# Performance work log

Hardware: AMD Instinct MI355X
Metric: run time of the kernel (lower is better)

## Reference

```python
import jax, jax.numpy as jnp
import numpy as np
from jax import lax

N, L, B = 256, 20, 10      # batch, max_seq (baskets), max_bas (items/basket)
D, H, ASP, K = 128, 128, 4, 16  # dim, h, aspects, nbNUM
NITEMS = 20000
H2 = 2 * H


def setup_inputs() -> dict:
    key = jax.random.key(0)
    ks = jax.random.split(key, 20)
    nrm = lambda k, shape, s=0.05: (jax.random.normal(k, shape) * s).astype(jnp.float32)
    seq = jax.random.randint(ks[0], (N, L, B), 0, NITEMS + 1)          # indices into itemEmb
    uHis = jax.random.uniform(ks[1], (N, NITEMS), dtype=jnp.float32)   # dense user history
    itemEmb = nrm(ks[2], (NITEMS + 1, D), 0.1).at[0].set(0.0)          # padding_idx=0 row zeroed
    fc1_w = nrm(ks[3], (1, L * B * D)); fc1_b = jnp.zeros((1,), jnp.float32)
    aspProju = nrm(ks[4], (ASP, 1, H))
    aspProji = nrm(ks[5], (ASP, D, H))
    dh_w = nrm(ks[6], (H, D)); dh_b = jnp.zeros((H,), jnp.float32)
    wih0 = nrm(ks[7], (4 * H2, H2)); whh0 = nrm(ks[8], (4 * H2, H2))
    bih0 = jnp.zeros((4 * H2,), jnp.float32); bhh0 = jnp.zeros((4 * H2,), jnp.float32)
    wih1 = nrm(ks[9], (4 * H2, H2)); whh1 = nrm(ks[10], (4 * H2, H2))
    bih1 = jnp.zeros((4 * H2,), jnp.float32); bhh1 = jnp.zeros((4 * H2,), jnp.float32)
    out_w = nrm(ks[11], (NITEMS, H2)); out_b = jnp.zeros((NITEMS,), jnp.float32)
    his_w = nrm(ks[12], (H2, NITEMS)); his_b = jnp.zeros((H2,), jnp.float32)
    g1_w = nrm(ks[13], (1, H2)); g1_b = jnp.zeros((1,), jnp.float32)
    g2_w = nrm(ks[14], (1, H2)); g2_b = jnp.zeros((1,), jnp.float32)
    return dict(seq=seq, uHis=uHis, itemEmb=itemEmb, fc1_w=fc1_w, fc1_b=fc1_b,
                aspProju=aspProju, aspProji=aspProji, dh_w=dh_w, dh_b=dh_b,
                wih0=wih0, whh0=whh0, bih0=bih0, bhh0=bhh0,
                wih1=wih1, whh1=whh1, bih1=bih1, bhh1=bhh1,
                out_w=out_w, out_b=out_b, his_w=his_w, his_b=his_b,
                g1_w=g1_w, g1_b=g1_b, g2_w=g2_w, g2_b=g2_b)


def _lstm_layer(x, wih, whh, bih, bhh):
    # x: [N, T, in]; PyTorch gate order i, f, g, o
    Hs = whh.shape[1]
    def step(carry, xt):
        h, c = carry
        g = xt @ wih.T + bih + h @ whh.T + bhh
        i, f, gg, o = jnp.split(g, 4, axis=-1)
        c = jax.nn.sigmoid(f) * c + jax.nn.sigmoid(i) * jnp.tanh(gg)
        h = jax.nn.sigmoid(o) * jnp.tanh(c)
        return (h, c), h
    h0 = jnp.zeros((x.shape[0], Hs), x.dtype)
    _, ys = lax.scan(step, (h0, h0), jnp.swapaxes(x, 0, 1))
    return jnp.swapaxes(ys, 0, 1)


def reference(seq, uHis, itemEmb, fc1_w, fc1_b, aspProju, aspProji, dh_w, dh_b,
              wih0, whh0, bih0, bhh0, wih1, whh1, bih1, bhh1,
              out_w, out_b, his_w, his_b, g1_w, g1_b, g2_w, g2_b):
    n, l, b = seq.shape
    embs = itemEmb[seq]                                   # [N,L,B,D]
    # MIE_user: fresh fc1 -> scalar per user, project per aspect
    u_embs = embs.reshape(n, -1) @ fc1_w.T + fc1_b        # [N,1]
    userAsp = jnp.tanh(jnp.einsum('no,aoh->nah', u_embs, aspProju))      # [N,ASP,H]
    # MIE_item
    itemAsp = jnp.tanh(jnp.einsum('nlbd,adh->nalbh', embs, aspProji))    # [N,ASP,L,B,H]
    # SNA: per-aspect exact L2 kNN over the batch (FAISS IndexFlatL2 equivalent)
    uA = jnp.transpose(jnp.tanh(userAsp), (1, 0, 2))      # [ASP,N,H] (double tanh, as in source)
    sq = jnp.sum(uA * uA, -1)                             # [ASP,N]
    dist = sq[:, :, None] + sq[:, None, :] - 2.0 * jnp.einsum('anh,amh->anm', uA, uA)
    dist = jnp.where(jnp.eye(n, dtype=bool)[None], -1.0, dist)   # self ranked first
    _, I = lax.top_k(lax.stop_gradient(-dist), K)         # [ASP,N,K] ascending distance
    I = I[:, :, 1:]                                       # drop self -> K-1 neighbors
    # sum of neighbor embeddings via multiplicity matmul (== gather+sum)
    M = jax.nn.one_hot(I, n, dtype=embs.dtype).sum(2)     # [ASP,N,N]
    nb_sum = jnp.einsum('apn,nlbd->aplbd', M, embs)       # [ASP,N,L,B,D]
    nb_h = nb_sum @ dh_w.T + dh_b                         # [ASP,N,L,B,H]
    embs_PI = jnp.transpose(nb_h.sum(axis=3), (1, 0, 2, 3))        # [N,ASP,L,H]
    embs_UI = jnp.tanh(itemAsp).sum(axis=3)               # [N,ASP,L,H] (double tanh)
    neighbAsps = jnp.concatenate([embs_UI, embs_PI], axis=-1)      # [N,ASP,L,2H]
    # raw view (not permute!) then max-pool over last dim of size ASP
    x = jnp.reshape(neighbAsps, (n, l, H2, ASP)).max(axis=-1)      # [N,L,2H]
    # 2-layer LSTM (eval mode: inter-layer dropout inactive)
    y = _lstm_layer(x, wih0, whh0, bih0, bhh0)
    y = _lstm_layer(y, wih1, whh1, bih1, bhh1)
    h_agg = jnp.tanh(y.sum(axis=1))                       # [N,2H]
    probs = jax.nn.softmax(h_agg @ out_w.T + out_b, axis=-1)       # [N,NITEMS]
    uHis_h = uHis @ his_w.T + his_b                        # [N,2H]
    gate = jax.nn.sigmoid(uHis_h @ g1_w.T + g1_b + h_agg @ g2_w.T + g2_b)  # [N,1]
    scores = gate * probs + (1.0 - gate) * uHis
    return scores
```

## Files before the change

kernel.cpp:

```cpp
#include <hip/hip_runtime.h>
#include <math.h>

#define N_ 256
#define L_ 20
#define B_ 10
#define D_ 128
#define H_ 128
#define ASP_ 4
#define KK_ 16
#define NIT_ 20000
#define H2_ 256
#define G4_ 1024
#define LBD_ 25600
#define NL_ 5120
#define NLB_ 51200

typedef __attribute__((ext_vector_type(8))) short bf16x8;
typedef __attribute__((ext_vector_type(4))) short bf16x4;
typedef __attribute__((ext_vector_type(4))) float f32x4;

__device__ __forceinline__ float sigf_fast(float x){
  return __builtin_amdgcn_rcpf(1.0f + __expf(-x));
}
__device__ __forceinline__ float tanh_fast(float x){
  return 1.0f - 2.0f*__builtin_amdgcn_rcpf(__expf(2.0f*x) + 1.0f);
}
__device__ __forceinline__ unsigned short f2b(float f){
  unsigned int u = __float_as_uint(f);
  unsigned int r = (u + 0x7FFFu + ((u>>16)&1u)) >> 16;
  return (unsigned short)r;
}
__device__ __forceinline__ float b2f(unsigned short b){
  return __uint_as_float(((unsigned int)b) << 16);
}

__global__ void k_gather2(const int* __restrict__ seq, const float* __restrict__ itemEmb,
                          float* __restrict__ embs, unsigned short* __restrict__ ebh,
                          float* __restrict__ eb){
  int nl = blockIdx.x;
  int d = threadIdx.x;
  float s = 0.f;
  #pragma unroll
  for(int b=0;b<B_;b++){
    int idx = seq[nl*B_ + b];
    float v = itemEmb[(size_t)idx*D_ + d];
    embs[(size_t)(nl*B_+b)*D_ + d] = v;
    ebh[(size_t)(nl*B_+b)*D_ + d] = f2b(v);
    s += v;
  }
  eb[(size_t)nl*D_ + d] = s;
}

__global__ void k_fc1(const float* __restrict__ embs, const float* __restrict__ w,
                      const float* __restrict__ b, float* __restrict__ u){
  int n = blockIdx.x; int t = threadIdx.x;
  float s = 0.f;
  for (int i = t; i < LBD_; i += 256) s += embs[n*LBD_+i]*w[i];
  __shared__ float red[256];
  red[t]=s; __syncthreads();
  for (int o=128;o>0;o>>=1){ if(t<o) red[t]+=red[t+o]; __syncthreads(); }
  if(t==0) u[n]=red[0]+b[0];
}

__global__ void k_uasq(const float* __restrict__ u, const float* __restrict__ proju,
                       float* __restrict__ ua, float* __restrict__ sq){
  int an = blockIdx.x;
  int h = threadIdx.x;
  int a = an / N_, n = an % N_;
  float v = tanhf(tanhf(u[n]*proju[a*H_+h]));
  ua[an*H_ + h] = v;
  __shared__ float red[128];
  red[h] = v*v; __syncthreads();
  for(int o=64;o>0;o>>=1){ if(h<o) red[h]+=red[h+o]; __syncthreads(); }
  if(h==0) sq[an]=red[0];
}

__global__ __launch_bounds__(256) void k_disttopk(const float* __restrict__ ua,
    const float* __restrict__ sq, int* __restrict__ nbr){
  int n = blockIdx.x, a = blockIdx.y, m = threadIdx.x;
  __shared__ float un[H_];
  __shared__ float row[N_];
  if(m < H_) un[m] = ua[(a*N_+n)*H_ + m];
  __syncthreads();
  const float* um = &ua[(a*N_+m)*H_];
  float dot=0.f;
  for(int h=0;h<H_;h++) dot += un[h]*um[h];
  float dval = sq[a*N_+n] + sq[a*N_+m] - 2.f*dot;
  if(m==n) dval = -1.0f;
  row[m] = dval;
  __syncthreads();
  if(m < 64){
    int lane = m;
    int wid = a*N_+n;
    float v[4]; int idx[4];
    #pragma unroll
    for(int j=0;j<4;j++){ int mm = lane*4 + j; v[j] = row[mm]; idx[j] = mm; }
    for(int k=0;k<KK_;k++){
      float bv = v[0]; int bi = idx[0];
      #pragma unroll
      for(int j=1;j<4;j++)
        if(v[j] < bv || (v[j]==bv && idx[j] < bi)){ bv=v[j]; bi=idx[j]; }
      float rv = bv; int ri = bi;
      #pragma unroll
      for(int o=32;o>0;o>>=1){
        float ov = __shfl_xor(rv, o, 64);
        int   oi = __shfl_xor(ri, o, 64);
        if(ov < rv || (ov==rv && oi < ri)){ rv=ov; ri=oi; }
      }
      if((ri>>2) == lane){ v[ri&3] = 3.4e38f; idx[ri&3] = 0x7fffffff; }
      if(k>0 && lane==0) nbr[wid*(KK_-1)+(k-1)] = ri;
    }
  }
}

__global__ void k_prep(const float* __restrict__ wih0, const float* __restrict__ whh0,
                       const float* __restrict__ wih1, const float* __restrict__ whh1,
                       const float* __restrict__ bih0, const float* __restrict__ bhh0,
                       const float* __restrict__ bih1, const float* __restrict__ bhh1,
                       const float* __restrict__ proji,
                       float* __restrict__ wp0, unsigned short* __restrict__ whb0,
                       float* __restrict__ wp1, unsigned short* __restrict__ whb1,
                       float* __restrict__ bp0, float* __restrict__ bp1,
                       unsigned short* __restrict__ projb){
  int i = blockIdx.x*blockDim.x + threadIdx.x;
  if(i < 262144){
    int k=i%H2_, j=i/H2_, g=j/H2_, jj=j%H2_;
    wp0[(jj*4+g)*H2_+k] = wih0[i];
  } else if(i < 524288){
    int e=i-262144; int k=e%H2_, j=e/H2_, g=j/H2_, jj=j%H2_;
    whb0[(jj*4+g)*H2_+k] = f2b(whh0[e]);
  } else if(i < 786432){
    int e=i-524288; int k=e%H2_, j=e/H2_, g=j/H2_, jj=j%H2_;
    wp1[(jj*4+g)*H2_+k] = wih1[e];
  } else if(i < 1048576){
    int e=i-786432; int k=e%H2_, j=e/H2_, g=j/H2_, jj=j%H2_;
    whb1[(jj*4+g)*H2_+k] = f2b(whh1[e]);
  } else if(i < 1114112){
    int e=i-1048576; int h=e%H_, d=(e/H_)%D_, aa=e/(D_*H_);
    projb[(aa*H_+h)*D_+d] = f2b(proji[e]);
  } else if(i < 1115136){
    int j=i-1114112; int g=j/H2_, jj=j%H2_;
    bp0[jj*4+g] = bih0[j] + bhh0[j];
  } else if(i < 1116160){
    int j=i-1115136; int g=j/H2_, jj=j%H2_;
    bp1[jj*4+g] = bih1[j] + bhh1[j];
  }
}

__global__ __launch_bounds__(256) void k_uimm(const unsigned short* __restrict__ ebh,
                                              const unsigned short* __restrict__ projb,
                                              float* __restrict__ na){
  __shared__ char smem[53248];
  unsigned short* As = (unsigned short*)smem;
  unsigned short* Bs = (unsigned short*)(smem + 20480);
  float*          Cs = (float*)smem;

  int mb = blockIdx.x;
  int a  = blockIdx.y;
  int tid = threadIdx.x;

  const unsigned short* asrc = ebh + (size_t)mb*10240;
  #pragma unroll
  for(int t=0;t<5;t++){
    int c = tid + t*256;
    int row = c >> 4;
    *(bf16x8*)(As + 8*(c ^ (row&7))) = *(const bf16x8*)(asrc + 8*c);
  }
  const unsigned short* bsrc = projb + a*16384;
  #pragma unroll
  for(int t=0;t<8;t++){
    int c = tid + t*256;
    int row = c >> 4;
    *(bf16x8*)(Bs + 8*(c ^ (row&7))) = *(const bf16x8*)(bsrc + 8*c);
  }
  __syncthreads();

  int lane = tid & 63, wave = tid >> 6;
  int l15 = lane & 15, l4 = lane >> 4;
  f32x4 acc[5][2] = {};
  #pragma unroll
  for(int kk=0;kk<4;kk++){
    bf16x8 bfr[2];
    #pragma unroll
    for(int tc=0;tc<2;tc++){
      int h = (wave*2+tc)*16 + l15;
      int c = h*16 + kk*4 + l4;
      bfr[tc] = *(const bf16x8*)(Bs + 8*(c ^ (h&7)));
    }
    #pragma unroll
    for(int tr=0;tr<5;tr++){
      int R = tr*16 + l15;
      int c = R*16 + kk*4 + l4;
      bf16x8 afr = *(const bf16x8*)(As + 8*(c ^ (R&7)));
      acc[tr][0] = __builtin_amdgcn_mfma_f32_16x16x32_bf16(afr, bfr[0], acc[tr][0], 0,0,0);
      acc[tr][1] = __builtin_amdgcn_mfma_f32_16x16x32_bf16(afr, bfr[1], acc[tr][1], 0,0,0);
    }
  }
  __syncthreads();

  #pragma unroll
  for(int tr=0;tr<5;tr++)
    #pragma unroll
    for(int tc=0;tc<2;tc++){
      int col = (wave*2+tc)*16 + l15;
      #pragma unroll
      for(int r=0;r<4;r++){
        int R = tr*16 + l4*4 + r;
        Cs[R*128 + col] = tanh_fast(tanh_fast(acc[tr][tc][r]));
      }
    }
  __syncthreads();

  #pragma unroll
  for(int t=0;t<4;t++){
    int oi = t*256 + tid;
    int g = oi >> 7, col = oi & 127;
    float s = 0.f;
    const float* p = Cs + g*1280 + col;
    #pragma unroll
    for(int b=0;b<10;b++) s += p[b*128];
    int nl = mb*8 + g;
    int n = nl/L_, l = nl%L_;
    na[((size_t)(n*ASP_+a)*L_ + l)*H2_ + col] = s;
  }
}

__global__ __launch_bounds__(256) void k_uhismm(const float* __restrict__ U,
    const float* __restrict__ W, const float* __restrict__ bias, float* __restrict__ C){
  __shared__ unsigned short As[2048];
  __shared__ unsigned short Bs[2048];
  int tid = threadIdx.x;
  int m0 = blockIdx.y*64, n0 = blockIdx.x*64;
  int kb0 = blockIdx.z*800;
  int row = tid & 63, q = tid >> 6;
  int lane = tid & 63, wave = tid >> 6;
  int l15 = lane & 15, l4 = lane >> 4;
  int wr = (wave>>1)*32, wc = (wave&1)*32;
  f32x4 acc[2][2] = {};
  for(int s=0;s<25;s++){
    int k0 = kb0 + s*32 + q*8;
    {
      const float* pa = &U[(size_t)(m0+row)*NIT_ + k0];
      float4 a0 = *(const float4*)pa, a1 = *(const float4*)(pa+4);
      bf16x8 av;
      av[0]=f2b(a0.x); av[1]=f2b(a0.y); av[2]=f2b(a0.z); av[3]=f2b(a0.w);
      av[4]=f2b(a1.x); av[5]=f2b(a1.y); av[6]=f2b(a1.z); av[7]=f2b(a1.w);
      *(bf16x8*)(As + 8*tid) = av;
      const float* pb = &W[(size_t)(n0+row)*NIT_ + k0];
      float4 b0 = *(const float4*)pb, b1 = *(const float4*)(pb+4);
      bf16x8 bv;
      bv[0]=f2b(b0.x); bv[1]=f2b(b0.y); bv[2]=f2b(b0.z); bv[3]=f2b(b0.w);
      bv[4]=f2b(b1.x); bv[5]=f2b(b1.y); bv[6]=f2b(b1.z); bv[7]=f2b(b1.w);
      *(bf16x8*)(Bs + 8*tid) = bv;
    }
    __syncthreads();
    bf16x8 afr[2], bfr[2];
    #pragma unroll
    for(int mt=0;mt<2;mt++) afr[mt] = *(const bf16x8*)(As + 8*(l4*64 + wr + mt*16 + l15));
    #pragma unroll
    for(int nt=0;nt<2;nt++) bfr[nt] = *(const bf16x8*)(Bs + 8*(l4*64 + wc + nt*16 + l15));
    #pragma unroll
    for(int mt=0;mt<2;mt++)
      #pragma unroll
      for(int nt=0;nt<2;nt++)
        acc[mt][nt] = __builtin_amdgcn_mfma_f32_16x16x32_bf16(afr[mt], bfr[nt], acc[mt][nt], 0,0,0);
    __syncthreads();
  }
  #pragma unroll
  for(int mt=0;mt<2;mt++)
    #pragma unroll
    for(int nt=0;nt<2;nt++){
      int col = n0 + wc + nt*16 + l15;
      #pragma unroll
      for(int r=0;r<4;r++){
        int rw = m0 + wr + mt*16 + l4*4 + r;
        float v = acc[mt][nt][r];
        if(blockIdx.z==0) v += bias[col];
        atomicAdd(&C[rw*H2_ + col], v);
      }
    }
}

__global__ __launch_bounds__(256) void k_xgmm(const float* __restrict__ A_,
    const float* __restrict__ W, const float* __restrict__ bias,
    unsigned short* __restrict__ Cb){
  __shared__ unsigned short As[2048];
  __shared__ unsigned short Bs[2048];
  int tid = threadIdx.x;
  int n0 = blockIdx.x*64, m0 = blockIdx.y*64;
  int row = tid & 63, q = tid >> 6;
  int lane = tid & 63, wave = tid >> 6;
  int l15 = lane & 15, l4 = lane >> 4;
  int wr = (wave>>1)*32, wc = (wave&1)*32;
  f32x4 acc[2][2] = {};
  for(int s=0;s<8;s++){
    int k0 = s*32 + q*8;
    {
      const float* pa = &A_[(size_t)(m0+row)*H2_ + k0];
      float4 a0 = *(const float4*)pa, a1 = *(const float4*)(pa+4);
      bf16x8 av;
      av[0]=f2b(a0.x); av[1]=f2b(a0.y); av[2]=f2b(a0.z); av[3]=f2b(a0.w);
      av[4]=f2b(a1.x); av[5]=f2b(a1.y); av[6]=f2b(a1.z); av[7]=f2b(a1.w);
      *(bf16x8*)(As + 8*tid) = av;
      const float* pb = &W[(size_t)(n0+row)*H2_ + k0];
      float4 b0 = *(const float4*)pb, b1 = *(const float4*)(pb+4);
      bf16x8 bv;
      bv[0]=f2b(b0.x); bv[1]=f2b(b0.y); bv[2]=f2b(b0.z); bv[3]=f2b(b0.w);
      bv[4]=f2b(b1.x); bv[5]=f2b(b1.y); bv[6]=f2b(b1.z); bv[7]=f2b(b1.w);
      *(bf16x8*)(Bs + 8*tid) = bv;
    }
    __syncthreads();
    bf16x8 afr[2], bfr[2];
    #pragma unroll
    for(int mt=0;mt<2;mt++) afr[mt] = *(const bf16x8*)(As + 8*(l4*64 + wr + mt*16 + l15));
    #pragma unroll
    for(int nt=0;nt<2;nt++) bfr[nt] = *(const bf16x8*)(Bs + 8*(l4*64 + wc + nt*16 + l15));
    #pragma unroll
    for(int mt=0;mt<2;mt++)
      #pragma unroll
      for(int nt=0;nt<2;nt++)
        acc[mt][nt] = __builtin_amdgcn_mfma_f32_16x16x32_bf16(afr[mt], bfr[nt], acc[mt][nt], 0,0,0);
    __syncthreads();
  }
  #pragma unroll
  for(int mt=0;mt<2;mt++)
    #pragma unroll
    for(int nt=0;nt<2;nt++){
      int col = n0 + wc + nt*16 + l15;
      float bs = bias[col];
      #pragma unroll
      for(int r=0;r<4;r++){
        int rw = m0 + wr + mt*16 + l4*4 + r;
        Cb[(size_t)rw*G4_ + col] = f2b(acc[mt][nt][r] + bs);
      }
    }
}

__global__ __launch_bounds__(256) void k_logitsmm(const unsigned short* __restrict__ Ab,
    const float* __restrict__ Wf, const float* __restrict__ bias,
    float* __restrict__ C){
  int n0 = blockIdx.x*32;
  int tid = threadIdx.x;
  int lane = tid & 63, wave = tid >> 6;
  int l15 = lane & 15, l4 = lane >> 4;
  f32x4 acc[4][2] = {};
  #pragma unroll
  for(int kk=0;kk<8;kk++){
    int k0 = kk*32 + l4*8;
    bf16x8 bfr[2];
    #pragma unroll
    for(int nt=0;nt<2;nt++){
      const float* pb = &Wf[(size_t)(n0 + nt*16 + l15)*H2_ + k0];
      float4 b0 = *(const float4*)pb, b1 = *(const float4*)(pb+4);
      bf16x8 bv;
      bv[0]=f2b(b0.x); bv[1]=f2b(b0.y); bv[2]=f2b(b0.z); bv[3]=f2b(b0.w);
      bv[4]=f2b(b1.x); bv[5]=f2b(b1.y); bv[6]=f2b(b1.z); bv[7]=f2b(b1.w);
      bfr[nt] = bv;
    }
    #pragma unroll
    for(int mt=0;mt<4;mt++){
      bf16x8 afr = *(const bf16x8*)(Ab + (size_t)(wave*64 + mt*16 + l15)*H2_ + k0);
      acc[mt][0] = __builtin_amdgcn_mfma_f32_16x16x32_bf16(afr, bfr[0], acc[mt][0], 0,0,0);
      acc[mt][1] = __builtin_amdgcn_mfma_f32_16x16x32_bf16(afr, bfr[1], acc[mt][1], 0,0,0);
    }
  }
  #pragma unroll
  for(int mt=0;mt<4;mt++)
    #pragma unroll
    for(int nt=0;nt<2;nt++){
      int col = n0 + nt*16 + l15;
      float bs = bias[col];
      #pragma unroll
      for(int r=0;r<4;r++){
        int row = wave*64 + mt*16 + l4*4 + r;
        C[(size_t)row*NIT_ + col] = acc[mt][nt][r] + bs;
      }
    }
}

__global__ __launch_bounds__(256) void k_gemm(const float* __restrict__ A, const float* __restrict__ W,
    float* __restrict__ C, const float* __restrict__ bias,
    int M, int Nn, int K, int kchunk, int atomic_mode){
  __shared__ float As[64][17];
  __shared__ float Ws[64][17];
  int tid = threadIdx.x;
  int tx = tid & 15, ty = tid >> 4;
  int m0 = blockIdx.y*64, n0 = blockIdx.x*64;
  int kb0 = blockIdx.z*kchunk;
  int kend = kb0 + kchunk; if(kend > K) kend = K;
  float acc[4][4] = {};
  int lrow = tid >> 2;
  int lc4 = (tid & 3) * 4;
  for(int kb = kb0; kb < kend; kb += 16){
    {
      int gr = m0 + lrow;
      float4 v = make_float4(0,0,0,0);
      if(gr < M) v = *(const float4*)&A[(long)gr*K + kb + lc4];
      As[lrow][lc4+0]=v.x; As[lrow][lc4+1]=v.y; As[lrow][lc4+2]=v.z; As[lrow][lc4+3]=v.w;
      int gw = n0 + lrow;
      float4 u = make_float4(0,0,0,0);
      if(gw < Nn) u = *(const float4*)&W[(long)gw*K + kb + lc4];
      Ws[lrow][lc4+0]=u.x; Ws[lrow][lc4+1]=u.y; Ws[lrow][lc4+2]=u.z; Ws[lrow][lc4+3]=u.w;
    }
    __syncthreads();
    for(int k=0;k<16;k++){
      float av[4], wv[4];
      #pragma unroll
      for(int r=0;r<4;r++) av[r]=As[ty*4+r][k];
      #pragma unroll
      for(int c=0;c<4;c++) wv[c]=Ws[tx*4+c][k];
      #pragma unroll
      for(int r=0;r<4;r++)
        #pragma unroll
        for(int c=0;c<4;c++) acc[r][c] += av[r]*wv[c];
    }
    __syncthreads();
  }
  for(int r=0;r<4;r++){
    int row = m0 + ty*4 + r; if(row >= M) continue;
    for(int c=0;c<4;c++){
      int col = n0 + tx*4 + c; if(col >= Nn) continue;
      float v = acc[r][c];
      if(bias && blockIdx.z==0) v += bias[col];
      if(atomic_mode) atomicAdd(&C[(long)row*Nn+col], v);
      else C[(long)row*Nn+col] = v;
    }
  }
}

__global__ void k_pi(const float* __restrict__ e2, const int* __restrict__ nbr,
                     const float* __restrict__ dh_b, float* __restrict__ na){
  int n = blockIdx.x, a = blockIdx.y, h = threadIdx.x;
  __shared__ int nb[KK_-1];
  if(h < KK_-1) nb[h] = nbr[(a*N_+n)*(KK_-1)+h];
  __syncthreads();
  float bias = (float)B_ * dh_b[h];
  for(int l=0;l<L_;l++){
    float s = bias;
    for(int k=0;k<KK_-1;k++) s += e2[(long)(nb[k]*L_ + l)*H_ + h];
    na[((long)(n*ASP_+a)*L_ + l)*H2_ + H_ + h] = s;
  }
}

__global__ void k_xmax(const float* __restrict__ na, float* __restrict__ x){
  int i = blockIdx.x*blockDim.x + threadIdx.x;
  if(i >= N_*L_*H2_) return;
  int n = i / (L_*H2_);
  int j = i % (L_*H2_);
  const float* p = &na[(long)n*ASP_*L_*H2_ + 4*j];
  x[i] = fmaxf(fmaxf(p[0],p[1]), fmaxf(p[2],p[3]));
}

__global__ __launch_bounds__(1024) void k_lstm_layer(
    const unsigned short* __restrict__ Whb,
    const unsigned short* __restrict__ xgb,
    float* __restrict__ Y){
  __shared__ unsigned short wc[65536];
  __shared__ unsigned short hs[2][16*H2_];
  int tid = threadIdx.x;
  int n0 = blockIdx.x * 16;
  int lane = tid & 63, wave = tid >> 6;
  int l15 = lane & 15, l4 = lane >> 4;
  int n = n0 + l15;
  float creg[4] = {0.f,0.f,0.f,0.f};
  {
    int ct0 = wave*4;
    #pragma unroll
    for(int it=0; it<8; it++){
      int c = it*64 + lane;
      int row = c >> 5;
      bf16x8 w8 = *(const bf16x8*)(Whb + (size_t)(ct0*16+row)*H2_ + (c&31)*8);
      *(bf16x8*)(wc + 8*((wave<<9) + (c ^ (row&7)))) = w8;
    }
  }
  const unsigned short* wptr[3];
  #pragma unroll
  for(int i=0;i<3;i++) wptr[i] = Whb + (size_t)((wave*4+1+i)*16 + l15)*H2_ + l4*8;
  const unsigned short* wc0 = wc + (wave<<12);
  __syncthreads();
  for(int t=0; t<L_; t++){
    bf16x4 xgv[4];
    #pragma unroll
    for(int i=0;i<4;i++){
      int jj = wave*16 + i*4 + l4;
      xgv[i] = *(const bf16x4*)(xgb + ((size_t)n*L_ + t)*G4_ + jj*4);
    }
    f32x4 acc[4] = {};
    if(t > 0){
      const unsigned short* hbuf = hs[(t+1)&1];
      bf16x8 hfr[8];
      #pragma unroll
      for(int kk=0; kk<8; kk++){
        int ch = l15*32 + kk*4 + l4;
        hfr[kk] = *(const bf16x8*)(hbuf + 8*(ch ^ (l15&7)));
      }
      #pragma unroll
      for(int kk=0; kk<8; kk++){
        bf16x8 wfr[4];
        wfr[0] = *(const bf16x8*)(wc0 + 8*((l15*32 + kk*4 + l4) ^ (l15&7)));
        #pragma unroll
        for(int i=0;i<3;i++) wfr[1+i] = *(const bf16x8*)(wptr[i] + kk*32);
        #pragma unroll
        for(int i=0;i<4;i++)
          acc[i] = __builtin_amdgcn_mfma_f32_16x16x32_bf16(wfr[i], hfr[kk], acc[i], 0,0,0);
      }
    }
    unsigned short* hout = hs[t&1];
    #pragma unroll
    for(int i=0;i<4;i++){
      int jj = wave*16 + i*4 + l4;
      float gi = acc[i][0] + b2f((unsigned short)xgv[i][0]);
      float gf = acc[i][1] + b2f((unsigned short)xgv[i][1]);
      float gg = acc[i][2] + b2f((unsigned short)xgv[i][2]);
      float go = acc[i][3] + b2f((unsigned short)xgv[i][3]);
      float cnew = sigf_fast(gf)*creg[i] + sigf_fast(gi)*tanh_fast(gg);
      creg[i] = cnew;
      float hnew = sigf_fast(go)*tanh_fast(cnew);
      Y[((size_t)n*L_ + t)*H2_ + jj] = hnew;
      int ch = l15*32 + (jj>>3);
      *(unsigned short*)((char*)hout + 16*(ch ^ (l15&7)) + (jj&7)*2) = f2b(hnew);
    }
    __syncthreads();
  }
}

__global__ void k_hagg_gate(const float* __restrict__ y1, const float* __restrict__ uhish,
                            const float* __restrict__ g1w, const float* __restrict__ g1b,
                            const float* __restrict__ g2w, const float* __restrict__ g2b,
                            float* __restrict__ hagg, unsigned short* __restrict__ haggb,
                            float* __restrict__ gate){
  int n = blockIdx.x; int jj = threadIdx.x;
  float s=0.f;
  for(int t=0;t<L_;t++) s += y1[((long)n*L_+t)*H2_ + jj];
  float v = tanhf(s);
  hagg[n*H2_+jj] = v;
  haggb[n*H2_+jj] = f2b(v);
  __shared__ float red[256];
  red[jj] = uhish[n*H2_+jj]*g1w[jj] + v*g2w[jj];
  __syncthreads();
  for(int o=128;o>0;o>>=1){ if(jj<o) red[jj]+=red[jj+o]; __syncthreads(); }
  if(jj==0) gate[n] = 1.f/(1.f+expf(-(red[0]+g1b[0]+g2b[0])));
}

__global__ __launch_bounds__(512) void k_softmax_out(const float* __restrict__ logits,
    const float* __restrict__ gate, const float* __restrict__ uHis, float* __restrict__ out){
  __shared__ float pe[NIT_];
  __shared__ float red[512];
  __shared__ float mm, ss;
  int n = blockIdx.x; int t = threadIdx.x;
  const float* row = &logits[(long)n*NIT_];
  float m = -3.4e38f;
  for(int i=t;i<NIT_;i+=512) m = fmaxf(m, row[i]);
  red[t]=m; __syncthreads();
  for(int o=256;o>0;o>>=1){ if(t<o) red[t]=fmaxf(red[t],red[t+o]); __syncthreads(); }
  if(t==0) mm = red[0];
  __syncthreads();
  float s=0.f;
  for(int i=t;i<NIT_;i+=512){
    float e = __expf(row[i]-mm);
    pe[i] = e;
    s += e;
  }
  __syncthreads();
  red[t]=s; __syncthreads();
  for(int o=256;o>0;o>>=1){ if(t<o) red[t]+=red[t+o]; __syncthreads(); }
  if(t==0) ss = red[0];
  __syncthreads();
  float g = gate[n];
  float* orow = out + (long)n*NIT_;
  const float* urow = uHis + (long)n*NIT_;
  for(int i=t;i<NIT_;i+=512){
    float p = pe[i]/ss;
    orow[i] = g*p + (1.f-g)*urow[i];
  }
}

extern "C" void kernel_launch(void* const* d_in, const int* in_sizes, int n_in,
                              void* d_out, int out_size, void* d_ws, size_t ws_size,
                              hipStream_t stream) {
  const int*   seq     = (const int*)  d_in[0];
  const float* uHis    = (const float*)d_in[1];
  const float* itemEmb = (const float*)d_in[2];
  const float* fc1_w   = (const float*)d_in[3];
  const float* fc1_b   = (const float*)d_in[4];
  const float* aspProju= (const float*)d_in[5];
  const float* aspProji= (const float*)d_in[6];
  const float* dh_w    = (const float*)d_in[7];
  const float* dh_b    = (const float*)d_in[8];
  const float* wih0    = (const float*)d_in[9];
  const float* whh0    = (const float*)d_in[10];
  const float* bih0    = (const float*)d_in[11];
  const float* bhh0    = (const float*)d_in[12];
  const float* wih1    = (const float*)d_in[13];
  const float* whh1    = (const float*)d_in[14];
  const float* bih1    = (const float*)d_in[15];
  const float* bhh1    = (const float*)d_in[16];
  const float* out_w   = (const float*)d_in[17];
  const float* out_b   = (const float*)d_in[18];
  const float* his_w   = (const float*)d_in[19];
  const float* his_b   = (const float*)d_in[20];
  const float* g1_w    = (const float*)d_in[21];
  const float* g1_b    = (const float*)d_in[22];
  const float* g2_w    = (const float*)d_in[23];
  const float* g2_b    = (const float*)d_in[24];

  float* ws = (float*)d_ws;
  float* embs = ws + 0;
  float* cub  = ws + 6553600;
  float* na   = ws + 13107200;
  float* x    = ws + 18350080;
  float* y0   = ws + 19660800;
  float* y1   = ws + 20971520;
  float* eb   = ws + 22282240;
  float* e2   = ws + 22937600;
  float* ua   = ws + 23855104;
  float* projT= ws + 23986176;
  float* wp0  = ws + 24051712;
  float* whp0 = ws + 24313856;
  float* wp1  = ws + 24576000;
  float* whp1 = ws + 24838144;
  float* bp0  = ws + 25100288;
  float* bp1  = ws + 25101312;
  float* uemb = ws + 25167872;
  float* sqb  = ws + 25168128;
  int*   nbr  = (int*)(ws + 25169152);
  float* uhish= ws + 25184512;
  float* hagg = ws + 25250048;
  float* gateb =ws + 25316096;
  float* logits = embs;
  unsigned short* ebh   = (unsigned short*)cub;
  unsigned short* xgb   = (unsigned short*)cub;
  unsigned short* projb = (unsigned short*)projT;
  unsigned short* haggb = (unsigned short*)x;
  unsigned short* whb0  = (unsigned short*)whp0;
  unsigned short* whb1  = (unsigned short*)whp1;

  k_gather2<<<NL_, D_, 0, stream>>>(seq, itemEmb, embs, ebh, eb);
  k_fc1<<<N_, 256, 0, stream>>>(embs, fc1_w, fc1_b, uemb);
  k_uasq<<<ASP_*N_, 128, 0, stream>>>(uemb, aspProju, ua, sqb);
  k_disttopk<<<dim3(N_,ASP_), 256, 0, stream>>>(ua, sqb, nbr);
  k_gemm<<<dim3(2, 80, 1), 256, 0, stream>>>(eb, dh_w, e2, nullptr, NL_, H_, D_, D_, 0);
  k_prep<<<4360, 256, 0, stream>>>(wih0, whh0, wih1, whh1, bih0, bhh0, bih1, bhh1,
                                   aspProji, wp0, whb0, wp1, whb1, bp0, bp1, projb);
  k_uimm<<<dim3(NL_/8, ASP_), 256, 0, stream>>>(ebh, projb, na);
  k_pi<<<dim3(N_,ASP_), H_, 0, stream>>>(e2, nbr, dh_b, na);
  k_xmax<<<(N_*L_*H2_+255)/256, 256, 0, stream>>>(na, x);
  k_xgmm<<<dim3(16,80), 256, 0, stream>>>(x, wp0, bp0, xgb);
  k_lstm_layer<<<16, 1024, 0, stream>>>(whb0, xgb, y0);
  k_xgmm<<<dim3(16,80), 256, 0, stream>>>(y0, wp1, bp1, xgb);
  k_lstm_layer<<<16, 1024, 0, stream>>>(whb1, xgb, y1);
  hipMemsetAsync(uhish, 0, N_*H2_*sizeof(float), stream);
  k_uhismm<<<dim3(4,4,25), 256, 0, stream>>>(uHis, his_w, his_b, uhish);
  k_hagg_gate<<<N_, 256, 0, stream>>>(y1, uhish, g1_w, g1_b, g2_w, g2_b, hagg, haggb, gateb);
  k_logitsmm<<<625, 256, 0, stream>>>(haggb, out_w, out_b, logits);
  k_softmax_out<<<N_, 512, 0, stream>>>(logits, gateb, uHis, (float*)d_out);
}
```

Measured before the change: 500.1 us.

## Co-schedule uHis GEMM with first LSTM layer and merge small prep kernels

Three launches are merged. The embedding gather and the weight-repack prep now run in one kernel, and the top-k neighbour search is fused with the neighbour-sum PI step. The main change runs the uHis projection GEMM in the same launch as the first LSTM layer, using spare blocks beside the 16 latency-bound recurrent blocks, so the HBM-heavy GEMM overlaps the sequential recurrence. This removes launch gaps and idle CUs, but the 144KB shared allocation per block may limit how the GEMM blocks co-reside.

```diff
diff --git a/kernel.cpp b/kernel.cpp
--- a/kernel.cpp
+++ b/kernel.cpp
@@ -34,21 +34,56 @@
   return __uint_as_float(((unsigned int)b) << 16);
 }
 
-__global__ void k_gather2(const int* __restrict__ seq, const float* __restrict__ itemEmb,
-                          float* __restrict__ embs, unsigned short* __restrict__ ebh,
-                          float* __restrict__ eb){
-  int nl = blockIdx.x;
-  int d = threadIdx.x;
-  float s = 0.f;
-  #pragma unroll
-  for(int b=0;b<B_;b++){
-    int idx = seq[nl*B_ + b];
-    float v = itemEmb[(size_t)idx*D_ + d];
-    embs[(size_t)(nl*B_+b)*D_ + d] = v;
-    ebh[(size_t)(nl*B_+b)*D_ + d] = f2b(v);
-    s += v;
-  }
-  eb[(size_t)nl*D_ + d] = s;
+__global__ __launch_bounds__(128) void k_gprep(const int* __restrict__ seq,
+    const float* __restrict__ itemEmb, float* __restrict__ embs,
+    unsigned short* __restrict__ ebh, float* __restrict__ eb,
+    const float* __restrict__ wih0, const float* __restrict__ whh0,
+    const float* __restrict__ wih1, const float* __restrict__ whh1,
+    const float* __restrict__ bih0, const float* __restrict__ bhh0,
+    const float* __restrict__ bih1, const float* __restrict__ bhh1,
+    const float* __restrict__ proji,
+    float* __restrict__ wp0, unsigned short* __restrict__ whb0,
+    float* __restrict__ wp1, unsigned short* __restrict__ whb1,
+    float* __restrict__ bp0, float* __restrict__ bp1,
+    unsigned short* __restrict__ projb){
+  if(blockIdx.x < NL_){
+    int nl = blockIdx.x;
+    int d = threadIdx.x;
+    float s = 0.f;
+    #pragma unroll
+    for(int b=0;b<B_;b++){
+      int idx = seq[nl*B_ + b];
+      float v = itemEmb[(size_t)idx*D_ + d];
+      embs[(size_t)(nl*B_+b)*D_ + d] = v;
+      ebh[(size_t)(nl*B_+b)*D_ + d] = f2b(v);
+      s += v;
+    }
+    eb[(size_t)nl*D_ + d] = s;
+  } else {
+    int i = (blockIdx.x - NL_)*128 + threadIdx.x;
+    if(i < 262144){
+      int k=i%H2_, j=i/H2_, g=j/H2_, jj=j%H2_;
+      wp0[(jj*4+g)*H2_+k] = wih0[i];
+    } else if(i < 524288){
+      int e=i-262144; int k=e%H2_, j=e/H2_, g=j/H2_, jj=j%H2_;
+      whb0[(jj*4+g)*H2_+k] = f2b(whh0[e]);
+    } else if(i < 786432){
+      int e=i-524288; int k=e%H2_, j=e/H2_, g=j/H2_, jj=j%H2_;
+      wp1[(jj*4+g)*H2_+k] = wih1[e];
+    } else if(i < 1048576){
+      int e=i-786432; int k=e%H2_, j=e/H2_, g=j/H2_, jj=j%H2_;
+      whb1[(jj*4+g)*H2_+k] = f2b(whh1[e]);
+    } else if(i < 1114112){
+      int e=i-1048576; int h=e%H_, d=(e/H_)%D_, aa=e/(D_*H_);
+      projb[(aa*H_+h)*D_+d] = f2b(proji[e]);
+    } else if(i < 1115136){
+      int j=i-1114112; int g=j/H2_, jj=j%H2_;
+      bp0[jj*4+g] = bih0[j] + bhh0[j];
+    } else if(i < 1116160){
+      int j=i-1115136; int g=j/H2_, jj=j%H2_;
+      bp1[jj*4+g] = bih1[j] + bhh1[j];
+    }
+  }
 }
 
 __global__ void k_fc1(const float* __restrict__ embs, const float* __restrict__ w,
@@ -75,11 +110,13 @@
   if(h==0) sq[an]=red[0];
 }
 
-__global__ __launch_bounds__(256) void k_disttopk(const float* __restrict__ ua,
-    const float* __restrict__ sq, int* __restrict__ nbr){
+__global__ __launch_bounds__(256) void k_disttopk_pi(const float* __restrict__ ua,
+    const float* __restrict__ sq, const float* __restrict__ e2,
+    const float* __restrict__ dh_b, int* __restrict__ nbr, float* __restrict__ na){
   int n = blockIdx.x, a = blockIdx.y, m = threadIdx.x;
   __shared__ float un[H_];
   __shared__ float row[N_];
+  __shared__ int nbs[KK_-1];
   if(m < H_) un[m] = ua[(a*N_+n)*H_ + m];
   __syncthreads();
   const float* um = &ua[(a*N_+m)*H_];
@@ -108,42 +145,18 @@
         if(ov < rv || (ov==rv && oi < ri)){ rv=ov; ri=oi; }
       }
       if((ri>>2) == lane){ v[ri&3] = 3.4e38f; idx[ri&3] = 0x7fffffff; }
-      if(k>0 && lane==0) nbr[wid*(KK_-1)+(k-1)] = ri;
-    }
-  }
-}
-
-__global__ void k_prep(const float* __restrict__ wih0, const float* __restrict__ whh0,
-                       const float* __restrict__ wih1, const float* __restrict__ whh1,
-                       const float* __restrict__ bih0, const float* __restrict__ bhh0,
-                       const float* __restrict__ bih1, const float* __restrict__ bhh1,
-                       const float* __restrict__ proji,
-                       float* __restrict__ wp0, unsigned short* __restrict__ whb0,
-                       float* __restrict__ wp1, unsigned short* __restrict__ whb1,
-                       float* __restrict__ bp0, float* __restrict__ bp1,
-                       unsigned short* __restrict__ projb){
-  int i = blockIdx.x*blockDim.x + threadIdx.x;
-  if(i < 262144){
-    int k=i%H2_, j=i/H2_, g=j/H2_, jj=j%H2_;
-    wp0[(jj*4+g)*H2_+k] = wih0[i];
-  } else if(i < 524288){
-    int e=i-262144; int k=e%H2_, j=e/H2_, g=j/H2_, jj=j%H2_;
-    whb0[(jj*4+g)*H2_+k] = f2b(whh0[e]);
-  } else if(i < 786432){
-    int e=i-524288; int k=e%H2_, j=e/H2_, g=j/H2_, jj=j%H2_;
-    wp1[(jj*4+g)*H2_+k] = wih1[e];
-  } else if(i < 1048576){
-    int e=i-786432; int k=e%H2_, j=e/H2_, g=j/H2_, jj=j%H2_;
-    whb1[(jj*4+g)*H2_+k] = f2b(whh1[e]);
-  } else if(i < 1114112){
-    int e=i-1048576; int h=e%H_, d=(e/H_)%D_, aa=e/(D_*H_);
-    projb[(aa*H_+h)*D_+d] = f2b(proji[e]);
-  } else if(i < 1115136){
-    int j=i-1114112; int g=j/H2_, jj=j%H2_;
-    bp0[jj*4+g] = bih0[j] + bhh0[j];
-  } else if(i < 1116160){
-    int j=i-1115136; int g=j/H2_, jj=j%H2_;
-    bp1[jj*4+g] = bih1[j] + bhh1[j];
+      if(k>0 && lane==0){ nbr[wid*(KK_-1)+(k-1)] = ri; nbs[k-1] = ri; }
+    }
+  }
+  __syncthreads();
+  if(m < H_){
+    int h = m;
+    float bias = (float)B_ * dh_b[h];
+    for(int l=0;l<L_;l++){
+      float s = bias;
+      for(int k=0;k<KK_-1;k++) s += e2[(size_t)(nbs[k]*L_ + l)*H_ + h];
+      na[((size_t)(n*ASP_+a)*L_ + l)*H2_ + H_ + h] = s;
+    }
   }
 }
 
@@ -223,62 +236,6 @@
     int n = nl/L_, l = nl%L_;
     na[((size_t)(n*ASP_+a)*L_ + l)*H2_ + col] = s;
   }
-}
-
-__global__ __launch_bounds__(256) void k_uhismm(const float* __restrict__ U,
-    const float* __restrict__ W, const float* __restrict__ bias, float* __restrict__ C){
-  __shared__ unsigned short As[2048];
-  __shared__ unsigned short Bs[2048];
-  int tid = threadIdx.x;
-  int m0 = blockIdx.y*64, n0 = blockIdx.x*64;
-  int kb0 = blockIdx.z*800;
-  int row = tid & 63, q = tid >> 6;
-  int lane = tid & 63, wave = tid >> 6;
-  int l15 = lane & 15, l4 = lane >> 4;
-  int wr = (wave>>1)*32, wc = (wave&1)*32;
-  f32x4 acc[2][2] = {};
-  for(int s=0;s<25;s++){
-    int k0 = kb0 + s*32 + q*8;
-    {
-      const float* pa = &U[(size_t)(m0+row)*NIT_ + k0];
-      float4 a0 = *(const float4*)pa, a1 = *(const float4*)(pa+4);
-      bf16x8 av;
-      av[0]=f2b(a0.x); av[1]=f2b(a0.y); av[2]=f2b(a0.z); av[3]=f2b(a0.w);
-      av[4]=f2b(a1.x); av[5]=f2b(a1.y); av[6]=f2b(a1.z); av[7]=f2b(a1.w);
-      *(bf16x8*)(As + 8*tid) = av;
-      const float* pb = &W[(size_t)(n0+row)*NIT_ + k0];
-      float4 b0 = *(const float4*)pb, b1 = *(const float4*)(pb+4);
-      bf16x8 bv;
-      bv[0]=f2b(b0.x); bv[1]=f2b(b0.y); bv[2]=f2b(b0.z); bv[3]=f2b(b0.w);
-      bv[4]=f2b(b1.x); bv[5]=f2b(b1.y); bv[6]=f2b(b1.z); bv[7]=f2b(b1.w);
-      *(bf16x8*)(Bs + 8*tid) = bv;
-    }
-    __syncthreads();
-    bf16x8 afr[2], bfr[2];
-    #pragma unroll
-    for(int mt=0;mt<2;mt++) afr[mt] = *(const bf16x8*)(As + 8*(l4*64 + wr + mt*16 + l15));
-    #pragma unroll
-    for(int nt=0;nt<2;nt++) bfr[nt] = *(const bf16x8*)(Bs + 8*(l4*64 + wc + nt*16 + l15));
-    #pragma unroll
-    for(int mt=0;mt<2;mt++)
-      #pragma unroll
-      for(int nt=0;nt<2;nt++)
-        acc[mt][nt] = __builtin_amdgcn_mfma_f32_16x16x32_bf16(afr[mt], bfr[nt], acc[mt][nt], 0,0,0);
-    __syncthreads();
-  }
-  #pragma unroll
-  for(int mt=0;mt<2;mt++)
-    #pragma unroll
-    for(int nt=0;nt<2;nt++){
-      int col = n0 + wc + nt*16 + l15;
-      #pragma unroll
-      for(int r=0;r<4;r++){
-        int rw = m0 + wr + mt*16 + l4*4 + r;
-        float v = acc[mt][nt][r];
-        if(blockIdx.z==0) v += bias[col];
-        atomicAdd(&C[rw*H2_ + col], v);
-      }
-    }
 }
 
 __global__ __launch_bounds__(256) void k_xgmm(const float* __restrict__ A_,
@@ -336,6 +293,213 @@
     }
 }
 
+__global__ __launch_bounds__(1024) void k_lstm0u(
+    const unsigned short* __restrict__ Whb, const unsigned short* __restrict__ xgb,
+    float* __restrict__ Y,
+    const float* __restrict__ U, const float* __restrict__ W,
+    const float* __restrict__ bias, float* __restrict__ C){
+  __shared__ char smem[147456];
+  int tid = threadIdx.x;
+  if(blockIdx.x < 16){
+    unsigned short* wc = (unsigned short*)smem;
+    char* hbase = smem + 131072;
+    int n0 = blockIdx.x * 16;
+    int lane = tid & 63, wave = tid >> 6;
+    int l15 = lane & 15, l4 = lane >> 4;
+    int n = n0 + l15;
+    float creg[4] = {0.f,0.f,0.f,0.f};
+    {
+      int ct0 = wave*4;
+      #pragma unroll
+      for(int it=0; it<8; it++){
+        int c = it*64 + lane;
+        int row = c >> 5;
+        bf16x8 w8 = *(const bf16x8*)(Whb + (size_t)(ct0*16+row)*H2_ + (c&31)*8);
+        *(bf16x8*)(wc + 8*((wave<<9) + (c ^ (row&7)))) = w8;
+      }
+    }
+    const unsigned short* wptr[3];
+    #pragma unroll
+    for(int i=0;i<3;i++) wptr[i] = Whb + (size_t)((wave*4+1+i)*16 + l15)*H2_ + l4*8;
+    const unsigned short* wc0 = wc + (wave<<12);
+    __syncthreads();
+    for(int t=0; t<L_; t++){
+      bf16x4 xgv[4];
+      #pragma unroll
+      for(int i=0;i<4;i++){
+        int jj = wave*16 + i*4 + l4;
+        xgv[i] = *(const bf16x4*)(xgb + ((size_t)n*L_ + t)*G4_ + jj*4);
+      }
+      f32x4 acc[4] = {};
+      if(t > 0){
+        const unsigned short* hbuf = (const unsigned short*)(hbase + ((t+1)&1)*8192);
+        bf16x8 hfr[8];
+        #pragma unroll
+        for(int kk=0; kk<8; kk++){
+          int ch = l15*32 + kk*4 + l4;
+          hfr[kk] = *(const bf16x8*)(hbuf + 8*(ch ^ (l15&7)));
+        }
+        #pragma unroll
+        for(int kk=0; kk<8; kk++){
+          bf16x8 wfr[4];
+          wfr[0] = *(const bf16x8*)(wc0 + 8*((l15*32 + kk*4 + l4) ^ (l15&7)));
+          #pragma unroll
+          for(int i=0;i<3;i++) wfr[1+i] = *(const bf16x8*)(wptr[i] + kk*32);
+          #pragma unroll
+          for(int i=0;i<4;i++)
+            acc[i] = __builtin_amdgcn_mfma_f32_16x16x32_bf16(wfr[i], hfr[kk], acc[i], 0,0,0);
+        }
+      }
+      char* hout = hbase + (t&1)*8192;
+      #pragma unroll
+      for(int i=0;i<4;i++){
+        int jj = wave*16 + i*4 + l4;
+        float gi = acc[i][0] + b2f((unsigned short)xgv[i][0]);
+        float gf = acc[i][1] + b2f((unsigned short)xgv[i][1]);
+        float gg = acc[i][2] + b2f((unsigned short)xgv[i][2]);
+        float go = acc[i][3] + b2f((unsigned short)xgv[i][3]);
+        float cnew = sigf_fast(gf)*creg[i] + sigf_fast(gi)*tanh_fast(gg);
+        creg[i] = cnew;
+        float hnew = sigf_fast(go)*tanh_fast(cnew);
+        Y[((size_t)n*L_ + t)*H2_ + jj] = hnew;
+        int ch = l15*32 + (jj>>3);
+        *(unsigned short*)(hout + 16*(ch ^ (l15&7)) + (jj&7)*2) = f2b(hnew);
+      }
+      __syncthreads();
+    }
+  } else {
+    int sub = tid >> 8;
+    int t2  = tid & 255;
+    int s_id = (blockIdx.x - 16)*4 + sub;
+    int n0 = (s_id & 3)*64;
+    int m0 = ((s_id>>2) & 3)*64;
+    int kz = s_id >> 4;
+    int kb0 = kz*800;
+    unsigned short* As = (unsigned short*)(smem + sub*8192);
+    unsigned short* Bs = (unsigned short*)(smem + sub*8192 + 4096);
+    int row = t2 & 63, q = t2 >> 6;
+    int lane = t2 & 63, wave = t2 >> 6;
+    int l15 = lane & 15, l4 = lane >> 4;
+    int wr = (wave>>1)*32, wc2 = (wave&1)*32;
+    f32x4 acc[2][2] = {};
+    for(int s=0;s<25;s++){
+      int k0 = kb0 + s*32 + q*8;
+      {
+        const float* pa = &U[(size_t)(m0+row)*NIT_ + k0];
+        float4 a0 = *(const float4*)pa, a1 = *(const float4*)(pa+4);
+        bf16x8 av;
+        av[0]=f2b(a0.x); av[1]=f2b(a0.y); av[2]=f2b(a0.z); av[3]=f2b(a0.w);
+        av[4]=f2b(a1.x); av[5]=f2b(a1.y); av[6]=f2b(a1.z); av[7]=f2b(a1.w);
+        *(bf16x8*)(As + 8*t2) = av;
+        const float* pb = &W[(size_t)(n0+row)*NIT_ + k0];
+        float4 b0 = *(const float4*)pb, b1 = *(const float4*)(pb+4);
+        bf16x8 bv;
+        bv[0]=f2b(b0.x); bv[1]=f2b(b0.y); bv[2]=f2b(b0.z); bv[3]=f2b(b0.w);
+        bv[4]=f2b(b1.x); bv[5]=f2b(b1.y); bv[6]=f2b(b1.z); bv[7]=f2b(b1.w);
+        *(bf16x8*)(Bs + 8*t2) = bv;
+      }
+      __syncthreads();
+      bf16x8 afr[2], bfr[2];
+      #pragma unroll
+      for(int mt=0;mt<2;mt++) afr[mt] = *(const bf16x8*)(As + 8*(l4*64 + wr + mt*16 + l15));
+      #pragma unroll
+      for(int nt=0;nt<2;nt++) bfr[nt] = *(const bf16x8*)(Bs + 8*(l4*64 + wc2 + nt*16 + l15));
+      #pragma unroll
+      for(int mt=0;mt<2;mt++)
+        #pragma unroll
+        for(int nt=0;nt<2;nt++)
+          acc[mt][nt] = __builtin_amdgcn_mfma_f32_16x16x32_bf16(afr[mt], bfr[nt], acc[mt][nt], 0,0,0);
+      __syncthreads();
+    }
+    #pragma unroll
+    for(int mt=0;mt<2;mt++)
+      #pragma unroll
+      for(int nt=0;nt<2;nt++){
+        int col = n0 + wc2 + nt*16 + l15;
+        #pragma unroll
+        for(int r=0;r<4;r++){
+          int rw = m0 + wr + mt*16 + l4*4 + r;
+          float v = acc[mt][nt][r];
+          if(kz==0) v += bias[col];
+          atomicAdd(&C[rw*H2_ + col], v);
+        }
+      }
+  }
+}
+
+__global__ __launch_bounds__(1024) void k_lstm_layer(
+    const unsigned short* __restrict__ Whb,
+    const unsigned short* __restrict__ xgb,
+    float* __restrict__ Y){
+  __shared__ unsigned short wc[65536];
+  __shared__ unsigned short hs[2][16*H2_];
+  int tid = threadIdx.x;
+  int n0 = blockIdx.x * 16;
+  int lane = tid & 63, wave = tid >> 6;
+  int l15 = lane & 15, l4 = lane >> 4;
+  int n = n0 + l15;
+  float creg[4] = {0.f,0.f,0.f,0.f};
+  {
+    int ct0 = wave*4;
+    #pragma unroll
+    for(int it=0; it<8; it++){
+      int c = it*64 + lane;
+      int row = c >> 5;
+      bf16x8 w8 = *(const bf16x8*)(Whb + (size_t)(ct0*16+row)*H2_ + (c&31)*8);
+      *(bf16x8*)(wc + 8*((wave<<9) + (c ^ (row&7)))) = w8;
+    }
+  }
+  const unsigned short* wptr[3];
+  #pragma unroll
+  for(int i=0;i<3;i++) wptr[i] = Whb + (size_t)((wave*4+1+i)*16 + l15)*H2_ + l4*8;
+  const unsigned short* wc0 = wc + (wave<<12);
+  __syncthreads();
+  for(int t=0; t<L_; t++){
+    bf16x4 xgv[4];
+    #pragma unroll
+    for(int i=0;i<4;i++){
+      int jj = wave*16 + i*4 + l4;
+      xgv[i] = *(const bf16x4*)(xgb + ((size_t)n*L_ + t)*G4_ + jj*4);
+    }
+    f32x4 acc[4] = {};
+    if(t > 0){
+      const unsigned short* hbuf = hs[(t+1)&1];
+      bf16x8 hfr[8];
+      #pragma unroll
+      for(int kk=0; kk<8; kk++){
+        int ch = l15*32 + kk*4 + l4;
+        hfr[kk] = *(const bf16x8*)(hbuf + 8*(ch ^ (l15&7)));
+      }
+      #pragma unroll
+      for(int kk=0; kk<8; kk++){
+        bf16x8 wfr[4];
+        wfr[0] = *(const bf16x8*)(wc0 + 8*((l15*32 + kk*4 + l4) ^ (l15&7)));
+        #pragma unroll
+        for(int i=0;i<3;i++) wfr[1+i] = *(const bf16x8*)(wptr[i] + kk*32);
+        #pragma unroll
+        for(int i=0;i<4;i++)
+          acc[i] = __builtin_amdgcn_mfma_f32_16x16x32_bf16(wfr[i], hfr[kk], acc[i], 0,0,0);
+      }
+    }
+    unsigned short* hout = hs[t&1];
+    #pragma unroll
+    for(int i=0;i<4;i++){
+      int jj = wave*16 + i*4 + l4;
+      float gi = acc[i][0] + b2f((unsigned short)xgv[i][0]);
+      float gf = acc[i][1] + b2f((unsigned short)xgv[i][1]);
+      float gg = acc[i][2] + b2f((unsigned short)xgv[i][2]);
+      float go = acc[i][3] + b2f((unsigned short)xgv[i][3]);
+      float cnew = sigf_fast(gf)*creg[i] + sigf_fast(gi)*tanh_fast(gg);
+      creg[i] = cnew;
+      float hnew = sigf_fast(go)*tanh_fast(cnew);
+      Y[((size_t)n*L_ + t)*H2_ + jj] = hnew;
+      int ch = l15*32 + (jj>>3);
+      *(unsigned short*)((char*)hout + 16*(ch ^ (l15&7)) + (jj&7)*2) = f2b(hnew);
+    }
+    __syncthreads();
+  }
+}
+
 __global__ __launch_bounds__(256) void k_logitsmm(const unsigned short* __restrict__ Ab,
     const float* __restrict__ Wf, const float* __restrict__ bias,
     float* __restrict__ C){
@@ -428,20 +592,6 @@
   }
 }
 
-__global__ void k_pi(const float* __restrict__ e2, const int* __restrict__ nbr,
-                     const float* __restrict__ dh_b, float* __restrict__ na){
-  int n = blockIdx.x, a = blockIdx.y, h = threadIdx.x;
-  __shared__ int nb[KK_-1];
-  if(h < KK_-1) nb[h] = nbr[(a*N_+n)*(KK_-1)+h];
-  __syncthreads();
-  float bias = (float)B_ * dh_b[h];
-  for(int l=0;l<L_;l++){
-    float s = bias;
-    for(int k=0;k<KK_-1;k++) s += e2[(long)(nb[k]*L_ + l)*H_ + h];
-    na[((long)(n*ASP_+a)*L_ + l)*H2_ + H_ + h] = s;
-  }
-}
-
 __global__ void k_xmax(const float* __restrict__ na, float* __restrict__ x){
   int i = blockIdx.x*blockDim.x + threadIdx.x;
   if(i >= N_*L_*H2_) return;
@@ -449,79 +599,6 @@
   int j = i % (L_*H2_);
   const float* p = &na[(long)n*ASP_*L_*H2_ + 4*j];
   x[i] = fmaxf(fmaxf(p[0],p[1]), fmaxf(p[2],p[3]));
-}
-
-__global__ __launch_bounds__(1024) void k_lstm_layer(
-    const unsigned short* __restrict__ Whb,
-    const unsigned short* __restrict__ xgb,
-    float* __restrict__ Y){
-  __shared__ unsigned short wc[65536];
-  __shared__ unsigned short hs[2][16*H2_];
-  int tid = threadIdx.x;
-  int n0 = blockIdx.x * 16;
-  int lane = tid & 63, wave = tid >> 6;
-  int l15 = lane & 15, l4 = lane >> 4;
-  int n = n0 + l15;
-  float creg[4] = {0.f,0.f,0.f,0.f};
-  {
-    int ct0 = wave*4;
-    #pragma unroll
-    for(int it=0; it<8; it++){
-      int c = it*64 + lane;
-      int row = c >> 5;
-      bf16x8 w8 = *(const bf16x8*)(Whb + (size_t)(ct0*16+row)*H2_ + (c&31)*8);
-      *(bf16x8*)(wc + 8*((wave<<9) + (c ^ (row&7)))) = w8;
-    }
-  }
-  const unsigned short* wptr[3];
-  #pragma unroll
-  for(int i=0;i<3;i++) wptr[i] = Whb + (size_t)((wave*4+1+i)*16 + l15)*H2_ + l4*8;
-  const unsigned short* wc0 = wc + (wave<<12);
-  __syncthreads();
-  for(int t=0; t<L_; t++){
-    bf16x4 xgv[4];
-    #pragma unroll
-    for(int i=0;i<4;i++){
-      int jj = wave*16 + i*4 + l4;
-      xgv[i] = *(const bf16x4*)(xgb + ((size_t)n*L_ + t)*G4_ + jj*4);
-    }
-    f32x4 acc[4] = {};
-    if(t > 0){
-      const unsigned short* hbuf = hs[(t+1)&1];
-      bf16x8 hfr[8];
-      #pragma unroll
-      for(int kk=0; kk<8; kk++){
-        int ch = l15*32 + kk*4 + l4;
-        hfr[kk] = *(const bf16x8*)(hbuf + 8*(ch ^ (l15&7)));
-      }
-      #pragma unroll
-      for(int kk=0; kk<8; kk++){
-        bf16x8 wfr[4];
-        wfr[0] = *(const bf16x8*)(wc0 + 8*((l15*32 + kk*4 + l4) ^ (l15&7)));
-        #pragma unroll
-        for(int i=0;i<3;i++) wfr[1+i] = *(const bf16x8*)(wptr[i] + kk*32);
-        #pragma unroll
-        for(int i=0;i<4;i++)
-          acc[i] = __builtin_amdgcn_mfma_f32_16x16x32_bf16(wfr[i], hfr[kk], acc[i], 0,0,0);
-      }
-    }
-    unsigned short* hout = hs[t&1];
-    #pragma unroll
-    for(int i=0;i<4;i++){
-      int jj = wave*16 + i*4 + l4;
-      float gi = acc[i][0] + b2f((unsigned short)xgv[i][0]);
-      float gf = acc[i][1] + b2f((unsigned short)xgv[i][1]);
-      float gg = acc[i][2] + b2f((unsigned short)xgv[i][2]);
-      float go = acc[i][3] + b2f((unsigned short)xgv[i][3]);
-      float cnew = sigf_fast(gf)*creg[i] + sigf_fast(gi)*tanh_fast(gg);
-      creg[i] = cnew;
-      float hnew = sigf_fast(go)*tanh_fast(cnew);
-      Y[((size_t)n*L_ + t)*H2_ + jj] = hnew;
-      int ch = l15*32 + (jj>>3);
-      *(unsigned short*)((char*)hout + 16*(ch ^ (l15&7)) + (jj&7)*2) = f2b(hnew);
-    }
-    __syncthreads();
-  }
 }
 
 __global__ void k_hagg_gate(const float* __restrict__ y1, const float* __restrict__ uhish,
@@ -635,22 +712,20 @@
   unsigned short* whb0  = (unsigned short*)whp0;
   unsigned short* whb1  = (unsigned short*)whp1;
 
-  k_gather2<<<NL_, D_, 0, stream>>>(seq, itemEmb, embs, ebh, eb);
+  k_gprep<<<NL_ + 8720, 128, 0, stream>>>(seq, itemEmb, embs, ebh, eb,
+      wih0, whh0, wih1, whh1, bih0, bhh0, bih1, bhh1, aspProji,
+      wp0, whb0, wp1, whb1, bp0, bp1, projb);
   k_fc1<<<N_, 256, 0, stream>>>(embs, fc1_w, fc1_b, uemb);
   k_uasq<<<ASP_*N_, 128, 0, stream>>>(uemb, aspProju, ua, sqb);
-  k_disttopk<<<dim3(N_,ASP_), 256, 0, stream>>>(ua, sqb, nbr);
   k_gemm<<<dim3(2, 80, 1), 256, 0, stream>>>(eb, dh_w, e2, nullptr, NL_, H_, D_, D_, 0);
-  k_prep<<<4360, 256, 0, stream>>>(wih0, whh0, wih1, whh1, bih0, bhh0, bih1, bhh1,
-                                   aspProji, wp0, whb0, wp1, whb1, bp0, bp1, projb);
+  k_disttopk_pi<<<dim3(N_,ASP_), 256, 0, stream>>>(ua, sqb, e2, dh_b, nbr, na);
   k_uimm<<<dim3(NL_/8, ASP_), 256, 0, stream>>>(ebh, projb, na);
-  k_pi<<<dim3(N_,ASP_), H_, 0, stream>>>(e2, nbr, dh_b, na);
   k_xmax<<<(N_*L_*H2_+255)/256, 256, 0, stream>>>(na, x);
   k_xgmm<<<dim3(16,80), 256, 0, stream>>>(x, wp0, bp0, xgb);
-  k_lstm_layer<<<16, 1024, 0, stream>>>(whb0, xgb, y0);
+  (void)hipMemsetAsync(uhish, 0, N_*H2_*sizeof(float), stream);
+  k_lstm0u<<<116, 1024, 0, stream>>>(whb0, xgb, y0, uHis, his_w, his_b, uhish);
   k_xgmm<<<dim3(16,80), 256, 0, stream>>>(y0, wp1, bp1, xgb);
   k_lstm_layer<<<16, 1024, 0, stream>>>(whb1, xgb, y1);
-  hipMemsetAsync(uhish, 0, N_*H2_*sizeof(float), stream);
-  k_uhismm<<<dim3(4,4,25), 256, 0, stream>>>(uHis, his_w, his_b, uhish);
   k_hagg_gate<<<N_, 256, 0, stream>>>(y1, uhish, g1_w, g1_b, g2_w, g2_b, hagg, haggb, gateb);
   k_logitsmm<<<625, 256, 0, stream>>>(haggb, out_w, out_b, logits);
   k_softmax_out<<<N_, 512, 0, stream>>>(logits, gateb, uHis, (float*)d_out);
```

Measured after the change: 465.7 us (median of 2 runs). 6.9% less time.
